# Performance work log

Measured on AMD Instinct MI355X. Metric: run time of the kernel, lower is better.

The kernel has to match this reference:

```python
import jax, jax.numpy as jnp
import numpy as np

B, N, E = 2, 2048, 2048
H, G, D = 16, 4, 128          # num_heads, num_kv_groups, head_dim = E // H
HID = 4 * E                    # GeGLU hidden width
EPS = 1e-6


def setup_inputs() -> dict:
    key = jax.random.key(0)
    ks = jax.random.split(key, 8)
    g = lambda k, shape: jax.random.normal(k, shape, jnp.float32) * 0.02
    return {
        "x": jax.random.normal(ks[0], (B, N, E), jnp.float32),
        "wq": g(ks[1], (E, H * D)),
        "wk": g(ks[2], (E, G * D)),
        "wv": g(ks[3], (E, G * D)),
        "wo": g(ks[4], (H * D, E)),
        "w1": g(ks[5], (E, 2 * HID)),   # GeGLU in-proj (value | gate)
        "w2": g(ks[6], (HID, E)),       # GeGLU out-proj
        "norm1_w": jnp.ones((E,), jnp.float32),
        "norm2_w": jnp.ones((E,), jnp.float32),
    }


def _rope_cos_sin(n, d, dtype):
    inv_freq = 1.0 / (10000.0 ** (jnp.arange(0, d, 2, dtype=jnp.float32) / d))
    freqs = jnp.arange(n, dtype=jnp.float32)[:, None] * inv_freq[None, :]  # [n, d/2]
    emb = jnp.concatenate([freqs, freqs], axis=-1)                          # [n, d]
    return jnp.cos(emb).astype(dtype), jnp.sin(emb).astype(dtype)


def _rotate_half(t):
    d2 = t.shape[-1] // 2
    return jnp.concatenate([-t[..., d2:], t[..., :d2]], axis=-1)


def _apply_rope(t, cos, sin):
    # t: [b, h, n, d]; cos/sin: [n, d]
    return t * cos + _rotate_half(t) * sin


def _rmsnorm(x, w):
    var = jnp.mean(jnp.square(x), axis=-1, keepdims=True)
    return x * jax.lax.rsqrt(var + EPS) * w


def reference(x, wq, wk, wv, wo, w1, w2, norm1_w, norm2_w):
    b, n, _ = x.shape
    # q = k = v = x reshaped into heads (pre-projection, as in source)
    qkv = x.reshape(b, n, H, D).transpose(0, 2, 1, 3)  # [b, H, n, D]
    cos, sin = _rope_cos_sin(n, D, x.dtype)
    q_r = _apply_rope(qkv, cos, sin)
    k_r = _apply_rope(qkv, cos, sin)
    # flatten back to [b, n, E]
    q_flat = q_r.transpose(0, 2, 1, 3).reshape(b, n, E)
    k_flat = k_r.transpose(0, 2, 1, 3).reshape(b, n, E)
    v_flat = x  # v untouched by RoPE; flatten == x

    # Grouped-query attention with internal projections
    qh = (q_flat @ wq).reshape(b, n, H, D).transpose(0, 2, 1, 3)       # [b, H, n, D]
    kh = (k_flat @ wk).reshape(b, n, G, D)                              # [b, n, G, D]
    vh = (v_flat @ wv).reshape(b, n, G, D)
    kh = jnp.repeat(kh, H // G, axis=2).transpose(0, 2, 1, 3)           # [b, H, n, D]
    vh = jnp.repeat(vh, H // G, axis=2).transpose(0, 2, 1, 3)

    scale = 1.0 / np.sqrt(D)
    scores = jnp.einsum('bhqd,bhkd->bhqk', qh, kh) * scale
    attn = jax.nn.softmax(scores, axis=-1)                               # [b, H, n, n]
    ctx = jnp.einsum('bhqk,bhkd->bhqd', attn, vh)
    attn_out = ctx.transpose(0, 2, 1, 3).reshape(b, n, H * D) @ wo      # [b, n, E]

    x1 = _rmsnorm(x + attn_out, norm1_w)

    # GeGLU FFN
    uv = x1 @ w1
    u, gate = jnp.split(uv, 2, axis=-1)
    fc = (u * jax.nn.gelu(gate)) @ w2

    x2 = _rmsnorm(x1 + fc, norm2_w)
    return (x2, (k_flat, v_flat), attn)
```

## Files before the change

### kernel.cpp

```cpp
#include <hip/hip_runtime.h>
#include <hip/hip_bf16.h>


using f32x4  = __attribute__((ext_vector_type(4))) float;
using bf16x8 = __attribute__((ext_vector_type(8))) short;
using bf16x4 = __attribute__((ext_vector_type(4))) short;
using u16x4  = __attribute__((ext_vector_type(4))) unsigned short;

#define DEV __device__ __forceinline__

#define ASYNC16(lds, g)                                                        \
  __builtin_amdgcn_global_load_lds(                                           \
      (const __attribute__((address_space(1))) void*)(g),                      \
      (__attribute__((address_space(3))) void*)(lds), 16, 0, 0)

DEV unsigned short f2bf(float f) {
  unsigned int u = __float_as_uint(f);
  return (unsigned short)((u + 0x7fffu + ((u >> 16) & 1u)) >> 16);
}
DEV float bf2f(unsigned short h) {
  return __uint_as_float(((unsigned int)h) << 16);
}

DEV float waveRedSum(float v) {
#pragma unroll
  for (int o = 32; o; o >>= 1) v += __shfl_xor(v, o);
  return v;
}

__global__ __launch_bounds__(256) void kconvAll(
    const float* __restrict__ wq, const float* __restrict__ wk,
    const float* __restrict__ wv, const float* __restrict__ wo,
    const float* __restrict__ w1, unsigned short* __restrict__ dst) {
  __shared__ float tile[32][33];
  int bx = blockIdx.x * 32;
  int by = blockIdx.y * 32;
  const float* src; int nsrc, c0;
  if (bx < 2048)      { src = wq; nsrc = 2048;  c0 = bx; }
  else if (bx < 2560) { src = wk; nsrc = 512;   c0 = bx - 2048; }
  else if (bx < 3072) { src = wv; nsrc = 512;   c0 = bx - 2560; }
  else if (bx < 5120) { src = wo; nsrc = 2048;  c0 = bx - 3072; }
  else                { src = w1; nsrc = 16384; c0 = bx - 5120; }
  int tx = threadIdx.x & 31;
  int ty = threadIdx.x >> 5;
#pragma unroll
  for (int i = 0; i < 32; i += 8)
    tile[ty + i][tx] = src[(size_t)(by + ty + i) * nsrc + c0 + tx];
  __syncthreads();
#pragma unroll
  for (int i = 0; i < 32; i += 8)
    dst[(size_t)(bx + ty + i) * 2048 + by + tx] = f2bf(tile[tx][ty + i]);
}

__global__ __launch_bounds__(256) void kconvT(const float* __restrict__ in,
                                              unsigned short* __restrict__ out,
                                              int K, int N) {
  __shared__ float tile[32][33];
  int bx = blockIdx.x * 32;
  int by = blockIdx.y * 32;
  int tx = threadIdx.x & 31;
  int ty = threadIdx.x >> 5;
#pragma unroll
  for (int i = 0; i < 32; i += 8)
    tile[ty + i][tx] = in[(size_t)(by + ty + i) * N + bx + tx];
  __syncthreads();
#pragma unroll
  for (int i = 0; i < 32; i += 8)
    out[(size_t)(bx + ty + i) * K + by + tx] = f2bf(tile[tx][ty + i]);
}

__global__ __launch_bounds__(256) void krope(const float* __restrict__ x,
                                             float* __restrict__ kout,
                                             float* __restrict__ vout,
                                             unsigned short* __restrict__ xq,
                                             unsigned short* __restrict__ xb) {
  int idx = blockIdx.x * 256 + threadIdx.x;
  int f  = idx & 63;
  int h  = (idx >> 6) & 15;
  int bn = idx >> 10;
  int n  = bn & 2047;
  size_t base = (size_t)bn * 2048 + h * 128;
  float inv = exp2f((float)f * (-13.287712379549449f / 64.0f));
  float ang = (float)n * inv;
  float c = cosf(ang), s = sinf(ang);
  float a = x[base + f], b = x[base + f + 64];
  float k1 = a * c - b * s;
  float k2 = b * c + a * s;
  __builtin_nontemporal_store(k1, kout + base + f);
  __builtin_nontemporal_store(k2, kout + base + f + 64);
  xq[base + f]      = f2bf(k1);
  xq[base + f + 64] = f2bf(k2);
  __builtin_nontemporal_store(a, vout + base + f);
  __builtin_nontemporal_store(b, vout + base + f + 64);
  xb[base + f]      = f2bf(a);
  xb[base + f + 64] = f2bf(b);
}

__global__ __launch_bounds__(256) void krms1(const float* __restrict__ x,
                                             const unsigned short* __restrict__ ao,
                                             const float* __restrict__ w,
                                             unsigned short* __restrict__ x1b) {
  size_t row = blockIdx.x;
  const f32x4* xp = (const f32x4*)(x + row * 2048);
  const u16x4* ap = (const u16x4*)(ao + row * 2048);
  int tid = threadIdx.x;
  f32x4 x0 = xp[tid * 2], x1v = xp[tid * 2 + 1];
  u16x4 a0 = ap[tid * 2], a1 = ap[tid * 2 + 1];
  f32x4 t0, t1;
#pragma unroll
  for (int i = 0; i < 4; ++i) {
    t0[i] = x0[i] + bf2f(a0[i]);
    t1[i] = x1v[i] + bf2f(a1[i]);
  }
  float ss = 0.f;
#pragma unroll
  for (int i = 0; i < 4; ++i) ss += t0[i] * t0[i] + t1[i] * t1[i];
  ss = waveRedSum(ss);
  __shared__ float red[4];
  int wid = tid >> 6, lane = tid & 63;
  if (!lane) red[wid] = ss;
  __syncthreads();
  ss = red[0] + red[1] + red[2] + red[3];
  float rr = rsqrtf(ss * (1.0f / 2048.0f) + 1e-6f);
  const f32x4* wp = (const f32x4*)w;
  f32x4 w0 = wp[tid * 2], w1 = wp[tid * 2 + 1];
  u16x4 o0, o1;
#pragma unroll
  for (int i = 0; i < 4; ++i) {
    o0[i] = f2bf(t0[i] * rr * w0[i]);
    o1[i] = f2bf(t1[i] * rr * w1[i]);
  }
  u16x4* op = (u16x4*)(x1b + row * 2048);
  op[tid * 2] = o0;
  op[tid * 2 + 1] = o1;
}

__global__ __launch_bounds__(256) void krms2(const unsigned short* __restrict__ x1b,
                                             const unsigned short* __restrict__ fc,
                                             const float* __restrict__ w,
                                             float* __restrict__ out) {
  size_t row = blockIdx.x;
  const u16x4* xp = (const u16x4*)(x1b + row * 2048);
  const u16x4* fp = (const u16x4*)(fc + row * 2048);
  int tid = threadIdx.x;
  u16x4 a0 = xp[tid * 2], a1 = xp[tid * 2 + 1];
  u16x4 b0 = fp[tid * 2], b1 = fp[tid * 2 + 1];
  f32x4 t0, t1;
#pragma unroll
  for (int i = 0; i < 4; ++i) {
    t0[i] = bf2f(a0[i]) + bf2f(b0[i]);
    t1[i] = bf2f(a1[i]) + bf2f(b1[i]);
  }
  float ss = 0.f;
#pragma unroll
  for (int i = 0; i < 4; ++i) ss += t0[i] * t0[i] + t1[i] * t1[i];
  ss = waveRedSum(ss);
  __shared__ float red[4];
  int wid = tid >> 6, lane = tid & 63;
  if (!lane) red[wid] = ss;
  __syncthreads();
  ss = red[0] + red[1] + red[2] + red[3];
  float rr = rsqrtf(ss * (1.0f / 2048.0f) + 1e-6f);
  const f32x4* wp = (const f32x4*)w;
  f32x4 w0 = wp[tid * 2], w1 = wp[tid * 2 + 1];
  f32x4* op = (f32x4*)(out + row * 2048);
  f32x4 o0 = t0 * rr * w0;
  f32x4 o1 = t1 * rr * w1;
  __builtin_nontemporal_store(o0, op + tid * 2);
  __builtin_nontemporal_store(o1, op + tid * 2 + 1);
}

__global__ __launch_bounds__(256, 2) void kvproj(
    const unsigned short* __restrict__ xq, const unsigned short* __restrict__ xb,
    const unsigned short* __restrict__ wkT, const unsigned short* __restrict__ wvT,
    unsigned short* __restrict__ kh, unsigned short* __restrict__ vhT) {
  const bool isV = blockIdx.z != 0;
  const unsigned short* A  = isV ? xb : xq;
  const unsigned short* Bt = isV ? wvT : wkT;
  __shared__ unsigned short As[2][128 * 32];
  __shared__ unsigned short Bs[2][128 * 32];
  const int tid = threadIdx.x;
  const int bm0 = blockIdx.y * 128, bn0 = blockIdx.x * 128;

  f32x4 acc[4][4] = {};

  const int lane = tid & 63, wid = tid >> 6;
  const int wr = wid >> 1, wc = wid & 1;
  const int lr = lane & 15, kq = lane >> 4;

  int srow[2], scc[2];
#pragma unroll
  for (int R = 0; R < 2; ++R) {
    int slot = R * 256 + tid;
    srow[R] = slot >> 2;
    scc[R]  = (slot & 3) ^ (srow[R] & 3);
  }
  auto stage = [&](int buf, int k0) {
#pragma unroll
    for (int R = 0; R < 2; ++R)
      ASYNC16(&As[buf][(R * 256 + tid) * 8],
              A + (size_t)(bm0 + srow[R]) * 2048 + k0 + scc[R] * 8);
#pragma unroll
    for (int R = 0; R < 2; ++R)
      ASYNC16(&Bs[buf][(R * 256 + tid) * 8],
              Bt + (size_t)(bn0 + srow[R]) * 2048 + k0 + scc[R] * 8);
  };

  const int NT = 64;
  stage(0, 0);
  stage(1, 32);
  int cur = 0;
  for (int t = 0; t < NT; ++t) {
    if (t + 1 < NT) asm volatile("s_waitcnt vmcnt(4)" ::: "memory");
    else            asm volatile("s_waitcnt vmcnt(0)" ::: "memory");
    __builtin_amdgcn_sched_barrier(0);
    __builtin_amdgcn_s_barrier();
    __builtin_amdgcn_sched_barrier(0);
    const unsigned short* Ac = As[cur];
    const unsigned short* Bc = Bs[cur];
    bf16x8 afr[4], bfr[4];
#pragma unroll
    for (int i = 0; i < 4; ++i) {
      int row = wr * 64 + i * 16 + lr;
      afr[i] = *(const bf16x8*)&Ac[row * 32 + ((kq ^ (row & 3)) * 8)];
    }
#pragma unroll
    for (int j = 0; j < 4; ++j) {
      int brow = wc * 64 + j * 16 + lr;
      bfr[j] = *(const bf16x8*)&Bc[brow * 32 + ((kq ^ (brow & 3)) * 8)];
    }
    asm volatile("s_waitcnt lgkmcnt(0)" ::: "memory");
    __builtin_amdgcn_sched_barrier(0);
    __builtin_amdgcn_s_barrier();
    __builtin_amdgcn_sched_barrier(0);
    if (t + 2 < NT) stage(cur, (t + 2) * 32);
    __builtin_amdgcn_s_setprio(1);
#pragma unroll
    for (int i = 0; i < 4; ++i)
#pragma unroll
      for (int j = 0; j < 4; ++j)
        acc[i][j] = __builtin_amdgcn_mfma_f32_16x16x32_bf16(afr[i], bfr[j],
                                                            acc[i][j], 0, 0, 0);
    __builtin_amdgcn_s_setprio(0);
    cur ^= 1;
  }

#pragma unroll
  for (int i = 0; i < 4; ++i)
#pragma unroll
    for (int j = 0; j < 4; ++j) {
      int rowb = bm0 + wr * 64 + i * 16 + kq * 4;
      int col = bn0 + wc * 64 + j * 16 + lr;
#pragma unroll
      for (int r = 0; r < 4; ++r) {
        unsigned short v = f2bf(acc[i][j][r]);
        if (isV) vhT[(size_t)col * 4096 + (rowb + r)] = v;
        else     kh[(size_t)(rowb + r) * 512 + col] = v;
      }
    }
}

__global__ __launch_bounds__(512, 4) void kattn(
    const unsigned short* __restrict__ qh,
    const unsigned short* __restrict__ kh,
    const unsigned short* __restrict__ vT,
    float* __restrict__ attn,
    unsigned short* __restrict__ ctx) {
  __shared__ __align__(16) char U[65536];
  __shared__ __align__(16) char Vb[16384];
  float* redm = (float*)Vb;
  float* reds = redm + 128;

  const int tid = threadIdx.x;
  const int lane = tid & 63, w = tid >> 6;
  const int lr = lane & 15, kq = lane >> 4;
  const int bid = blockIdx.x;
  const int g8 = bid & 7;
  const int j  = bid >> 3;
  const int bz = g8 >> 2;
  const int gz = g8 & 3;
  const int hz = gz * 4 + (j & 3);
  const int q0 = (j >> 2) << 4;
  const int z  = bz * 16 + hz;

  const unsigned short* Aq =
      qh + ((size_t)(bz * 2048 + q0 + lr) * 2048 + hz * 128);
  bf16x8 qfr[4];
#pragma unroll
  for (int kk = 0; kk < 4; ++kk)
    qfr[kk] = *(const bf16x8*)(Aq + kk * 32 + kq * 8);

  const unsigned short* Kb =
      kh + ((size_t)(bz * 2048) * 512 + gz * 128);
  int krow[4], kcs[4];
#pragma unroll
  for (int R = 0; R < 4; ++R) {
    int idx = R * 64 + lane;
    krow[R] = idx >> 4;
    kcs[R] = (idx & 15) ^ (krow[R] & 7);
  }
  auto stageK = [&](int buf, int t) {
#pragma unroll
    for (int R = 0; R < 4; ++R)
      ASYNC16(U + buf * 32768 + w * 4096 + (R * 64 + lane) * 16,
              Kb + (size_t)(t * 128 + w * 16 + krow[R]) * 512 + kcs[R] * 8);
  };

  f32x4 acc[16];
#pragma unroll
  for (int t = 0; t < 16; ++t) acc[t] = f32x4{0.f, 0.f, 0.f, 0.f};

  stageK(0, 0);
  stageK(1, 1);
#pragma unroll
  for (int t = 0; t < 16; ++t) {
    if (t < 15) asm volatile("s_waitcnt vmcnt(4)" ::: "memory");
    else        asm volatile("s_waitcnt vmcnt(0)" ::: "memory");
    __builtin_amdgcn_sched_barrier(0);
    const char* Kw = U + (t & 1) * 32768 + w * 4096;
    bf16x8 kfr[4];
#pragma unroll
    for (int kk = 0; kk < 4; ++kk) {
      int cch = (kk * 4 + kq) ^ (lr & 7);
      kfr[kk] = *(const bf16x8*)(Kw + lr * 256 + cch * 16);
    }
    asm volatile("s_waitcnt lgkmcnt(0)" ::: "memory");
    __builtin_amdgcn_sched_barrier(0);
    if (t + 2 < 16) stageK(t & 1, t + 2);
    __builtin_amdgcn_s_setprio(1);
#pragma unroll
    for (int kk = 0; kk < 4; ++kk)
      acc[t] = __builtin_amdgcn_mfma_f32_16x16x32_bf16(kfr[kk], qfr[kk],
                                                       acc[t], 0, 0, 0);
    __builtin_amdgcn_s_setprio(0);
  }

  const float scale = 0.08838834764831845f;
  float mx = -3.4e38f;
#pragma unroll
  for (int t = 0; t < 16; ++t) {
    acc[t] *= scale;
#pragma unroll
    for (int r = 0; r < 4; ++r) mx = fmaxf(mx, acc[t][r]);
  }
  mx = fmaxf(mx, __shfl_xor(mx, 16));
  mx = fmaxf(mx, __shfl_xor(mx, 32));
  float sm = 0.f;
#pragma unroll
  for (int t = 0; t < 16; ++t) {
#pragma unroll
    for (int r = 0; r < 4; ++r) {
      float e = __expf(acc[t][r] - mx);
      acc[t][r] = e;
      sm += e;
    }
  }
  sm += __shfl_xor(sm, 16);
  sm += __shfl_xor(sm, 32);
  if (kq == 0) { redm[w * 16 + lr] = mx; reds[w * 16 + lr] = sm; }
  __syncthreads();
  float m = redm[lr];
#pragma unroll
  for (int ww = 1; ww < 8; ++ww) m = fmaxf(m, redm[ww * 16 + lr]);
  float s = 0.f;
#pragma unroll
  for (int ww = 0; ww < 8; ++ww)
    s += reds[ww * 16 + lr] * __expf(redm[ww * 16 + lr] - m);
  float invw = __expf(mx - m) / s;

  float* arow = attn + (((size_t)z * 2048 + q0 + lr) * 2048);
#pragma unroll
  for (int t = 0; t < 16; ++t) {
    int key = t * 128 + w * 16 + kq * 4;
    f32x4 p = acc[t] * invw;
    __builtin_nontemporal_store(p, (f32x4*)(arow + key));
    bf16x4 pb;
#pragma unroll
    for (int r = 0; r < 4; ++r) pb[r] = (short)f2bf(p[r]);
    int c8 = key >> 3;
    *(bf16x4*)(U + lr * 4096 + ((c8 ^ (lr & 7)) << 4) + ((key & 7) << 1)) = pb;
  }
  __syncthreads();

  const unsigned short* Bv = vT + (size_t)gz * 524288 + bz * 2048;
  const int d0 = w * 16;
  const int vd = lane >> 2;
  const int vcs = (lane & 3) ^ (vd & 3);
  auto stageV = [&](int buf, int t) {
    ASYNC16(Vb + buf * 8192 + w * 1024 + lane * 16,
            Bv + (size_t)(d0 + vd) * 4096 + t * 32 + vcs * 8);
  };

  f32x4 cfr = {};
  stageV(0, 0);
  stageV(1, 1);
#pragma unroll
  for (int t = 0; t < 64; ++t) {
    if (t < 63) asm volatile("s_waitcnt vmcnt(1)" ::: "memory");
    else        asm volatile("s_waitcnt vmcnt(0)" ::: "memory");
    __builtin_amdgcn_sched_barrier(0);
    int c8 = t * 4 + kq;
    bf16x8 pfr = *(const bf16x8*)(U + lr * 4096 + ((c8 ^ (lr & 7)) << 4));
    const char* Vw = Vb + (t & 1) * 8192 + w * 1024;
    bf16x8 vfr = *(const bf16x8*)(Vw + lr * 64 + ((kq ^ (lr & 3)) << 4));
    asm volatile("s_waitcnt lgkmcnt(0)" ::: "memory");
    __builtin_amdgcn_sched_barrier(0);
    if (t + 2 < 64) stageV(t & 1, t + 2);
    __builtin_amdgcn_s_setprio(1);
    cfr = __builtin_amdgcn_mfma_f32_16x16x32_bf16(pfr, vfr, cfr, 0, 0, 0);
    __builtin_amdgcn_s_setprio(0);
  }
#pragma unroll
  for (int r = 0; r < 4; ++r) {
    int q = kq * 4 + r;
    ctx[((size_t)(bz * 2048 + q0 + q) * 2048) + hz * 128 + d0 + lr] =
        f2bf(cfr[r]);
  }
}

template <bool OUT_BF16>
__global__ __launch_bounds__(512, 2) void gemm128(
    const unsigned short* __restrict__ A, const unsigned short* __restrict__ Bt,
    void* __restrict__ C_, int K, int lda, int ldb, int ldc) {
  __shared__ unsigned short As[2][128 * 64];
  __shared__ unsigned short Bs[2][128 * 64];
  const int tid = threadIdx.x;
  const int bid = blockIdx.x;
  const int xcd = bid & 7, ii = bid >> 3;
  const int my = (xcd >> 1) * 8 + (ii & 7);
  const int nx = (xcd & 1) * 8 + (ii >> 3);
  const int bm0 = my * 128, bn0 = nx * 128;
  const int lane = tid & 63, wid = tid >> 6;
  const int wr = wid >> 2, wc = wid & 3;
  const int lr = lane & 15, kq = lane >> 4;

  f32x4 acc[4][2] = {};

  int sArow[2], sAcc[2];
#pragma unroll
  for (int R = 0; R < 2; ++R) {
    int c = R * 512 + tid;
    sArow[R] = c >> 3;
    sAcc[R]  = (c & 7) ^ (sArow[R] & 7);
  }

  auto stage = [&](int buf, int k0) {
#pragma unroll
    for (int R = 0; R < 2; ++R)
      ASYNC16(&As[buf][(R * 512 + tid) * 8],
              A + (size_t)(bm0 + sArow[R]) * lda + k0 + sAcc[R] * 8);
#pragma unroll
    for (int R = 0; R < 2; ++R)
      ASYNC16(&Bs[buf][(R * 512 + tid) * 8],
              Bt + (size_t)(bn0 + sArow[R]) * ldb + k0 + sAcc[R] * 8);
  };

  const int NT = K >> 6;
  stage(0, 0);
  stage(1, 64);
  int cur = 0;
  for (int t = 0; t < NT; ++t) {
    if (t + 1 < NT) asm volatile("s_waitcnt vmcnt(4)" ::: "memory");
    else            asm volatile("s_waitcnt vmcnt(0)" ::: "memory");
    __builtin_amdgcn_sched_barrier(0);
    __builtin_amdgcn_s_barrier();
    __builtin_amdgcn_sched_barrier(0);
    const unsigned short* Ac = As[cur];
    const unsigned short* Bc = Bs[cur];
    bf16x8 afr0[4], bfr0[2];
#pragma unroll
    for (int i = 0; i < 4; ++i) {
      int row = wr * 64 + i * 16 + lr;
      afr0[i] = *(const bf16x8*)&Ac[(row * 8 + (kq ^ (row & 7))) * 8];
    }
#pragma unroll
    for (int j2 = 0; j2 < 2; ++j2) {
      int brow = wc * 32 + j2 * 16 + lr;
      bfr0[j2] = *(const bf16x8*)&Bc[(brow * 8 + (kq ^ (brow & 7))) * 8];
    }
    __builtin_amdgcn_s_setprio(1);
#pragma unroll
    for (int j2 = 0; j2 < 2; ++j2)
#pragma unroll
      for (int i = 0; i < 4; ++i)
        acc[i][j2] = __builtin_amdgcn_mfma_f32_16x16x32_bf16(afr0[i], bfr0[j2],
                                                             acc[i][j2], 0, 0, 0);
    __builtin_amdgcn_s_setprio(0);
    bf16x8 afr1[4], bfr1[2];
#pragma unroll
    for (int i = 0; i < 4; ++i) {
      int row = wr * 64 + i * 16 + lr;
      afr1[i] = *(const bf16x8*)&Ac[(row * 8 + ((4 + kq) ^ (row & 7))) * 8];
    }
#pragma unroll
    for (int j2 = 0; j2 < 2; ++j2) {
      int brow = wc * 32 + j2 * 16 + lr;
      bfr1[j2] = *(const bf16x8*)&Bc[(brow * 8 + ((4 + kq) ^ (brow & 7))) * 8];
    }
    asm volatile("s_waitcnt lgkmcnt(0)" ::: "memory");
    __builtin_amdgcn_sched_barrier(0);
    __builtin_amdgcn_s_barrier();
    __builtin_amdgcn_sched_barrier(0);
    if (t + 2 < NT) stage(cur, (t + 2) << 6);
    __builtin_amdgcn_s_setprio(1);
#pragma unroll
    for (int j2 = 0; j2 < 2; ++j2)
#pragma unroll
      for (int i = 0; i < 4; ++i)
        acc[i][j2] = __builtin_amdgcn_mfma_f32_16x16x32_bf16(afr1[i], bfr1[j2],
                                                             acc[i][j2], 0, 0, 0);
    __builtin_amdgcn_s_setprio(0);
    cur ^= 1;
  }

#pragma unroll
  for (int i = 0; i < 4; ++i)
#pragma unroll
    for (int j = 0; j < 2; ++j) {
      int rowb = bm0 + wr * 64 + i * 16 + kq * 4;
      int col = bn0 + wc * 32 + j * 16 + lr;
#pragma unroll
      for (int r = 0; r < 4; ++r) {
        if constexpr (OUT_BF16)
          ((unsigned short*)C_)[(size_t)(rowb + r) * ldc + col] = f2bf(acc[i][j][r]);
        else
          ((float*)C_)[(size_t)(rowb + r) * ldc + col] = acc[i][j][r];
      }
    }
}

__global__ __launch_bounds__(512, 2) void gemm_geglu256(
    const unsigned short* __restrict__ A, const unsigned short* __restrict__ B1,
    const unsigned short* __restrict__ B2, unsigned short* __restrict__ H_,
    int K, int lda, int ldb, int ldc) {
  __shared__ unsigned short As[2][256 * 64];
  __shared__ unsigned short B1s[2][128 * 64];
  __shared__ unsigned short B2s[2][128 * 64];
  const int tid = threadIdx.x;
  const int bid = blockIdx.x;
  const int xcd = bid & 7, ii = bid >> 3;
  const int my = (xcd >> 2) * 8 + (ii & 7);
  const int nx = (xcd & 3) * 16 + (ii >> 3);
  const int bm0 = my * 256, bn0 = nx * 128;
  const int lane = tid & 63, wid = tid >> 6;
  const int wr = wid >> 2, wc = wid & 3;
  const int lr = lane & 15, kq = lane >> 4;

  f32x4 accu[8][2] = {};
  f32x4 accg[8][2] = {};

  int sArow[4], sAcc[4], sBrow[2], sBcc[2];
#pragma unroll
  for (int R = 0; R < 4; ++R) {
    int c = R * 512 + tid;
    sArow[R] = c >> 3;
    sAcc[R]  = (c & 7) ^ (sArow[R] & 7);
  }
#pragma unroll
  for (int R = 0; R < 2; ++R) {
    int c = R * 512 + tid;
    sBrow[R] = c >> 3;
    sBcc[R]  = (c & 7) ^ (sBrow[R] & 7);
  }

  auto stage = [&](int buf, int k0) {
#pragma unroll
    for (int R = 0; R < 4; ++R)
      ASYNC16(&As[buf][(R * 512 + tid) * 8],
              A + (size_t)(bm0 + sArow[R]) * lda + k0 + sAcc[R] * 8);
#pragma unroll
    for (int R = 0; R < 2; ++R)
      ASYNC16(&B1s[buf][(R * 512 + tid) * 8],
              B1 + (size_t)(bn0 + sBrow[R]) * ldb + k0 + sBcc[R] * 8);
#pragma unroll
    for (int R = 0; R < 2; ++R)
      ASYNC16(&B2s[buf][(R * 512 + tid) * 8],
              B2 + (size_t)(bn0 + sBrow[R]) * ldb + k0 + sBcc[R] * 8);
  };

  const int NT = K >> 6;
  stage(0, 0);
  stage(1, 64);
  int cur = 0;
  for (int t = 0; t < NT; ++t) {
    if (t + 1 < NT) asm volatile("s_waitcnt vmcnt(8)" ::: "memory");
    else            asm volatile("s_waitcnt vmcnt(0)" ::: "memory");
    __builtin_amdgcn_sched_barrier(0);
    __builtin_amdgcn_s_barrier();
    __builtin_amdgcn_sched_barrier(0);
    const unsigned short* Ac = As[cur];
    const unsigned short* B1c = B1s[cur];
    const unsigned short* B2c = B2s[cur];
    bf16x8 afr0[8], b10[2], b20[2];
#pragma unroll
    for (int i = 0; i < 8; ++i) {
      int row = wr * 128 + i * 16 + lr;
      afr0[i] = *(const bf16x8*)&Ac[(row * 8 + (kq ^ (row & 7))) * 8];
    }
#pragma unroll
    for (int j2 = 0; j2 < 2; ++j2) {
      int brow = wc * 32 + j2 * 16 + lr;
      b10[j2] = *(const bf16x8*)&B1c[(brow * 8 + (kq ^ (brow & 7))) * 8];
      b20[j2] = *(const bf16x8*)&B2c[(brow * 8 + (kq ^ (brow & 7))) * 8];
    }
    __builtin_amdgcn_s_setprio(1);
#pragma unroll
    for (int j2 = 0; j2 < 2; ++j2)
#pragma unroll
      for (int i = 0; i < 8; ++i) {
        accu[i][j2] = __builtin_amdgcn_mfma_f32_16x16x32_bf16(afr0[i], b10[j2],
                                                              accu[i][j2], 0, 0, 0);
        accg[i][j2] = __builtin_amdgcn_mfma_f32_16x16x32_bf16(afr0[i], b20[j2],
                                                              accg[i][j2], 0, 0, 0);
      }
    __builtin_amdgcn_s_setprio(0);
    bf16x8 afr1[8], b11[2], b21[2];
#pragma unroll
    for (int i = 0; i < 8; ++i) {
      int row = wr * 128 + i * 16 + lr;
      afr1[i] = *(const bf16x8*)&Ac[(row * 8 + ((4 + kq) ^ (row & 7))) * 8];
    }
#pragma unroll
    for (int j2 = 0; j2 < 2; ++j2) {
      int brow = wc * 32 + j2 * 16 + lr;
      b11[j2] = *(const bf16x8*)&B1c[(brow * 8 + ((4 + kq) ^ (brow & 7))) * 8];
      b21[j2] = *(const bf16x8*)&B2c[(brow * 8 + ((4 + kq) ^ (brow & 7))) * 8];
    }
    asm volatile("s_waitcnt lgkmcnt(0)" ::: "memory");
    __builtin_amdgcn_sched_barrier(0);
    __builtin_amdgcn_s_barrier();
    __builtin_amdgcn_sched_barrier(0);
    if (t + 2 < NT) stage(cur, (t + 2) << 6);
    __builtin_amdgcn_s_setprio(1);
#pragma unroll
    for (int j2 = 0; j2 < 2; ++j2)
#pragma unroll
      for (int i = 0; i < 8; ++i) {
        accu[i][j2] = __builtin_amdgcn_mfma_f32_16x16x32_bf16(afr1[i], b11[j2],
                                                              accu[i][j2], 0, 0, 0);
        accg[i][j2] = __builtin_amdgcn_mfma_f32_16x16x32_bf16(afr1[i], b21[j2],
                                                              accg[i][j2], 0, 0, 0);
      }
    __builtin_amdgcn_s_setprio(0);
    cur ^= 1;
  }

#pragma unroll
  for (int i = 0; i < 8; ++i)
#pragma unroll
    for (int j = 0; j < 2; ++j) {
      int rowb = bm0 + wr * 128 + i * 16 + kq * 4;
      int col = bn0 + wc * 32 + j * 16 + lr;
#pragma unroll
      for (int r = 0; r < 4; ++r) {
        float u = accu[i][j][r];
        float g = accg[i][j][r];
        float tv = tanhf(0.7978845608028654f * (g + 0.044715f * g * g * g));
        float hv = u * 0.5f * g * (1.0f + tv);
        H_[(size_t)(rowb + r) * ldc + col] = f2bf(hv);
      }
    }
}

extern "C" void kernel_launch(void* const* d_in, const int* in_sizes, int n_in,
                              void* d_out, int out_size, void* d_ws, size_t ws_size,
                              hipStream_t stream) {
  const float* x   = (const float*)d_in[0];
  const float* wq  = (const float*)d_in[1];
  const float* wk  = (const float*)d_in[2];
  const float* wv  = (const float*)d_in[3];
  const float* wo  = (const float*)d_in[4];
  const float* w1  = (const float*)d_in[5];
  const float* w2  = (const float*)d_in[6];
  const float* n1w = (const float*)d_in[7];
  const float* n2w = (const float*)d_in[8];

  float* out    = (float*)d_out;
  float* x2_out = out;
  float* k_out  = out + 8388608;
  float* v_out  = out + 16777216;
  float* attn   = out + 25165824;

  char* ws = (char*)d_ws;
  unsigned short* wqT  = (unsigned short*)(ws + 0);
  unsigned short* wkT  = (unsigned short*)(ws + 8388608);
  unsigned short* wvT  = (unsigned short*)(ws + 10485760);
  unsigned short* woT  = (unsigned short*)(ws + 12582912);
  unsigned short* w1T  = (unsigned short*)(ws + 20971520);
  unsigned short* w2T  = (unsigned short*)(ws + 88080384);
  unsigned short* qh   = (unsigned short*)(ws + 121634816);
  unsigned short* kh   = (unsigned short*)(ws + 138412032);
  unsigned short* vhT  = (unsigned short*)(ws + 142606336);
  unsigned short* ctx  = (unsigned short*)(ws + 146800640);
  unsigned short* aob  = (unsigned short*)(ws + 163577856);
  unsigned short* hbuf = (unsigned short*)(ws + 121634816);
  unsigned short* x1b  = (unsigned short*)(ws + 197132288);
  unsigned short* fc   = (unsigned short*)(ws + 213909504);

  unsigned short* xb = (unsigned short*)attn;
  unsigned short* xq = xb + 8388608;

  dim3 blk(256);
  dim3 blk512(512);

  kconvAll<<<dim3(672, 64), blk, 0, stream>>>(wq, wk, wv, wo, w1, wqT);
  kconvT<<<dim3(64, 256), blk, 0, stream>>>(w2, w2T, 8192, 2048);

  krope<<<16384, blk, 0, stream>>>(x, k_out, v_out, xq, xb);

  gemm128<true><<<dim3(512), blk512, 0, stream>>>(
      xq, wqT, qh, 2048, 2048, 2048, 2048);
  kvproj<<<dim3(4, 32, 2), blk, 0, stream>>>(xq, xb, wkT, wvT, kh, vhT);

  kattn<<<dim3(4096), blk512, 0, stream>>>(qh, kh, vhT, attn, ctx);

  gemm128<true><<<dim3(512), blk512, 0, stream>>>(
      ctx, woT, aob, 2048, 2048, 2048, 2048);
  krms1<<<4096, blk, 0, stream>>>(x, aob, n1w, x1b);
  gemm_geglu256<<<dim3(1024), blk512, 0, stream>>>(
      x1b, w1T, w1T + 16777216, hbuf, 2048, 2048, 2048, 8192);
  gemm128<true><<<dim3(512), blk512, 0, stream>>>(
      hbuf, w2T, fc, 8192, 8192, 8192, 2048);
  krms2<<<4096, blk, 0, stream>>>(x1b, fc, n2w, x2_out);
}
```

Before: 905.0 us.

## Merge weight conversion and RoPE kernels; fuse Q/K/V projections into one GEMM

The weight transpose/convert kernels and the RoPE kernel are merged into one launch that dispatches on block index. The Q projection (formerly gemm128) and the K/V projection are merged into a single 768-block GEMM kernel with 512 threads, a 64-wide K tile and an XCD-aware tile mapping for the Q part. The aim is to cut launch overhead and fill the GPU better, because the small K/V GEMM now runs alongside the Q GEMM instead of after it. The risk is that the fused GEMM uses a different tiling from the tuned gemm128, and that the larger LDS footprint may lower occupancy.

```diff
diff --git a/kernel.cpp b/kernel.cpp
--- a/kernel.cpp
+++ b/kernel.cpp
@@ -28,72 +28,69 @@
   return v;
 }
 
-__global__ __launch_bounds__(256) void kconvAll(
+__global__ __launch_bounds__(256) void kprep(
     const float* __restrict__ wq, const float* __restrict__ wk,
     const float* __restrict__ wv, const float* __restrict__ wo,
-    const float* __restrict__ w1, unsigned short* __restrict__ dst) {
+    const float* __restrict__ w1, const float* __restrict__ w2,
+    unsigned short* __restrict__ dst, unsigned short* __restrict__ w2T,
+    const float* __restrict__ x, float* __restrict__ kout,
+    float* __restrict__ vout, unsigned short* __restrict__ xq,
+    unsigned short* __restrict__ xb) {
   __shared__ float tile[32][33];
-  int bx = blockIdx.x * 32;
-  int by = blockIdx.y * 32;
-  const float* src; int nsrc, c0;
-  if (bx < 2048)      { src = wq; nsrc = 2048;  c0 = bx; }
-  else if (bx < 2560) { src = wk; nsrc = 512;   c0 = bx - 2048; }
-  else if (bx < 3072) { src = wv; nsrc = 512;   c0 = bx - 2560; }
-  else if (bx < 5120) { src = wo; nsrc = 2048;  c0 = bx - 3072; }
-  else                { src = w1; nsrc = 16384; c0 = bx - 5120; }
-  int tx = threadIdx.x & 31;
-  int ty = threadIdx.x >> 5;
-#pragma unroll
-  for (int i = 0; i < 32; i += 8)
-    tile[ty + i][tx] = src[(size_t)(by + ty + i) * nsrc + c0 + tx];
-  __syncthreads();
-#pragma unroll
-  for (int i = 0; i < 32; i += 8)
-    dst[(size_t)(bx + ty + i) * 2048 + by + tx] = f2bf(tile[tx][ty + i]);
-}
-
-__global__ __launch_bounds__(256) void kconvT(const float* __restrict__ in,
-                                              unsigned short* __restrict__ out,
-                                              int K, int N) {
-  __shared__ float tile[32][33];
-  int bx = blockIdx.x * 32;
-  int by = blockIdx.y * 32;
-  int tx = threadIdx.x & 31;
-  int ty = threadIdx.x >> 5;
-#pragma unroll
-  for (int i = 0; i < 32; i += 8)
-    tile[ty + i][tx] = in[(size_t)(by + ty + i) * N + bx + tx];
-  __syncthreads();
-#pragma unroll
-  for (int i = 0; i < 32; i += 8)
-    out[(size_t)(bx + ty + i) * K + by + tx] = f2bf(tile[tx][ty + i]);
-}
-
-__global__ __launch_bounds__(256) void krope(const float* __restrict__ x,
-                                             float* __restrict__ kout,
-                                             float* __restrict__ vout,
-                                             unsigned short* __restrict__ xq,
-                                             unsigned short* __restrict__ xb) {
-  int idx = blockIdx.x * 256 + threadIdx.x;
-  int f  = idx & 63;
-  int h  = (idx >> 6) & 15;
-  int bn = idx >> 10;
-  int n  = bn & 2047;
-  size_t base = (size_t)bn * 2048 + h * 128;
-  float inv = exp2f((float)f * (-13.287712379549449f / 64.0f));
-  float ang = (float)n * inv;
-  float c = cosf(ang), s = sinf(ang);
-  float a = x[base + f], b = x[base + f + 64];
-  float k1 = a * c - b * s;
-  float k2 = b * c + a * s;
-  __builtin_nontemporal_store(k1, kout + base + f);
-  __builtin_nontemporal_store(k2, kout + base + f + 64);
-  xq[base + f]      = f2bf(k1);
-  xq[base + f + 64] = f2bf(k2);
-  __builtin_nontemporal_store(a, vout + base + f);
-  __builtin_nontemporal_store(b, vout + base + f + 64);
-  xb[base + f]      = f2bf(a);
-  xb[base + f + 64] = f2bf(b);
+  const int bidg = blockIdx.x;
+  if (bidg < 43008) {
+    int bx = (bidg % 672) * 32;
+    int by = (bidg / 672) * 32;
+    const float* src; int nsrc, c0;
+    if (bx < 2048)      { src = wq; nsrc = 2048;  c0 = bx; }
+    else if (bx < 2560) { src = wk; nsrc = 512;   c0 = bx - 2048; }
+    else if (bx < 3072) { src = wv; nsrc = 512;   c0 = bx - 2560; }
+    else if (bx < 5120) { src = wo; nsrc = 2048;  c0 = bx - 3072; }
+    else                { src = w1; nsrc = 16384; c0 = bx - 5120; }
+    int tx = threadIdx.x & 31;
+    int ty = threadIdx.x >> 5;
+#pragma unroll
+    for (int i = 0; i < 32; i += 8)
+      tile[ty + i][tx] = src[(size_t)(by + ty + i) * nsrc + c0 + tx];
+    __syncthreads();
+#pragma unroll
+    for (int i = 0; i < 32; i += 8)
+      dst[(size_t)(bx + ty + i) * 2048 + by + tx] = f2bf(tile[tx][ty + i]);
+  } else if (bidg < 59392) {
+    int l = bidg - 43008;
+    int bx = (l & 63) * 32;
+    int by = (l >> 6) * 32;
+    int tx = threadIdx.x & 31;
+    int ty = threadIdx.x >> 5;
+#pragma unroll
+    for (int i = 0; i < 32; i += 8)
+      tile[ty + i][tx] = w2[(size_t)(by + ty + i) * 2048 + bx + tx];
+    __syncthreads();
+#pragma unroll
+    for (int i = 0; i < 32; i += 8)
+      w2T[(size_t)(bx + ty + i) * 8192 + by + tx] = f2bf(tile[tx][ty + i]);
+  } else {
+    int idx = (bidg - 59392) * 256 + threadIdx.x;
+    int f  = idx & 63;
+    int h  = (idx >> 6) & 15;
+    int bn = idx >> 10;
+    int n  = bn & 2047;
+    size_t base = (size_t)bn * 2048 + h * 128;
+    float inv = exp2f((float)f * (-13.287712379549449f / 64.0f));
+    float ang = (float)n * inv;
+    float c = cosf(ang), s = sinf(ang);
+    float a = x[base + f], b = x[base + f + 64];
+    float k1 = a * c - b * s;
+    float k2 = b * c + a * s;
+    __builtin_nontemporal_store(k1, kout + base + f);
+    __builtin_nontemporal_store(k2, kout + base + f + 64);
+    xq[base + f]      = f2bf(k1);
+    xq[base + f + 64] = f2bf(k2);
+    __builtin_nontemporal_store(a, vout + base + f);
+    __builtin_nontemporal_store(b, vout + base + f + 64);
+    xb[base + f]      = f2bf(a);
+    xb[base + f + 64] = f2bf(b);
+  }
 }
 
 __global__ __launch_bounds__(256) void krms1(const float* __restrict__ x,
@@ -170,45 +167,61 @@
   __builtin_nontemporal_store(o1, op + tid * 2 + 1);
 }
 
-__global__ __launch_bounds__(256, 2) void kvproj(
+__global__ __launch_bounds__(512, 2) void qkvgemm(
     const unsigned short* __restrict__ xq, const unsigned short* __restrict__ xb,
-    const unsigned short* __restrict__ wkT, const unsigned short* __restrict__ wvT,
+    const unsigned short* __restrict__ wqT, const unsigned short* __restrict__ wkT,
+    const unsigned short* __restrict__ wvT, unsigned short* __restrict__ qh,
     unsigned short* __restrict__ kh, unsigned short* __restrict__ vhT) {
-  const bool isV = blockIdx.z != 0;
-  const unsigned short* A  = isV ? xb : xq;
-  const unsigned short* Bt = isV ? wvT : wkT;
-  __shared__ unsigned short As[2][128 * 32];
-  __shared__ unsigned short Bs[2][128 * 32];
+  __shared__ unsigned short As[2][128 * 64];
+  __shared__ unsigned short Bs[2][128 * 64];
   const int tid = threadIdx.x;
-  const int bm0 = blockIdx.y * 128, bn0 = blockIdx.x * 128;
-
-  f32x4 acc[4][4] = {};
-
+  const int bid = blockIdx.x;
+  const unsigned short *A, *Bt;
+  int bm0, bn0, mode;
+  if (bid < 512) {
+    const int xcd = bid & 7, ii = bid >> 3;
+    bm0 = ((xcd >> 1) * 8 + (ii & 7)) * 128;
+    bn0 = ((xcd & 1) * 8 + (ii >> 3)) * 128;
+    A = xq; Bt = wqT; mode = 0;
+  } else if (bid < 640) {
+    int l = bid - 512;
+    bm0 = (l >> 2) * 128;
+    bn0 = (l & 3) * 128;
+    A = xq; Bt = wkT; mode = 1;
+  } else {
+    int l = bid - 640;
+    bm0 = (l >> 2) * 128;
+    bn0 = (l & 3) * 128;
+    A = xb; Bt = wvT; mode = 2;
+  }
   const int lane = tid & 63, wid = tid >> 6;
-  const int wr = wid >> 1, wc = wid & 1;
+  const int wr = wid >> 2, wc = wid & 3;
   const int lr = lane & 15, kq = lane >> 4;
 
-  int srow[2], scc[2];
+  f32x4 acc[4][2] = {};
+
+  int sArow[2], sAcc[2];
 #pragma unroll
   for (int R = 0; R < 2; ++R) {
-    int slot = R * 256 + tid;
-    srow[R] = slot >> 2;
-    scc[R]  = (slot & 3) ^ (srow[R] & 3);
-  }
+    int c = R * 512 + tid;
+    sArow[R] = c >> 3;
+    sAcc[R]  = (c & 7) ^ (sArow[R] & 7);
+  }
+
   auto stage = [&](int buf, int k0) {
 #pragma unroll
     for (int R = 0; R < 2; ++R)
-      ASYNC16(&As[buf][(R * 256 + tid) * 8],
-              A + (size_t)(bm0 + srow[R]) * 2048 + k0 + scc[R] * 8);
+      ASYNC16(&As[buf][(R * 512 + tid) * 8],
+              A + (size_t)(bm0 + sArow[R]) * 2048 + k0 + sAcc[R] * 8);
 #pragma unroll
     for (int R = 0; R < 2; ++R)
-      ASYNC16(&Bs[buf][(R * 256 + tid) * 8],
-              Bt + (size_t)(bn0 + srow[R]) * 2048 + k0 + scc[R] * 8);
+      ASYNC16(&Bs[buf][(R * 512 + tid) * 8],
+              Bt + (size_t)(bn0 + sArow[R]) * 2048 + k0 + sAcc[R] * 8);
   };
 
-  const int NT = 64;
+  const int NT = 32;
   stage(0, 0);
-  stage(1, 32);
+  stage(1, 64);
   int cur = 0;
   for (int t = 0; t < NT; ++t) {
     if (t + 1 < NT) asm volatile("s_waitcnt vmcnt(4)" ::: "memory");
@@ -218,29 +231,48 @@
     __builtin_amdgcn_sched_barrier(0);
     const unsigned short* Ac = As[cur];
     const unsigned short* Bc = Bs[cur];
-    bf16x8 afr[4], bfr[4];
+    bf16x8 afr0[4], bfr0[2];
 #pragma unroll
     for (int i = 0; i < 4; ++i) {
       int row = wr * 64 + i * 16 + lr;
-      afr[i] = *(const bf16x8*)&Ac[row * 32 + ((kq ^ (row & 3)) * 8)];
-    }
-#pragma unroll
-    for (int j = 0; j < 4; ++j) {
-      int brow = wc * 64 + j * 16 + lr;
-      bfr[j] = *(const bf16x8*)&Bc[brow * 32 + ((kq ^ (brow & 3)) * 8)];
+      afr0[i] = *(const bf16x8*)&Ac[(row * 8 + (kq ^ (row & 7))) * 8];
+    }
+#pragma unroll
+    for (int j2 = 0; j2 < 2; ++j2) {
+      int brow = wc * 32 + j2 * 16 + lr;
+      bfr0[j2] = *(const bf16x8*)&Bc[(brow * 8 + (kq ^ (brow & 7))) * 8];
+    }
+    __builtin_amdgcn_s_setprio(1);
+#pragma unroll
+    for (int j2 = 0; j2 < 2; ++j2)
+#pragma unroll
+      for (int i = 0; i < 4; ++i)
+        acc[i][j2] = __builtin_amdgcn_mfma_f32_16x16x32_bf16(afr0[i], bfr0[j2],
+                                                             acc[i][j2], 0, 0, 0);
+    __builtin_amdgcn_s_setprio(0);
+    bf16x8 afr1[4], bfr1[2];
+#pragma unroll
+    for (int i = 0; i < 4; ++i) {
+      int row = wr * 64 + i * 16 + lr;
+      afr1[i] = *(const bf16x8*)&Ac[(row * 8 + ((4 + kq) ^ (row & 7))) * 8];
+    }
+#pragma unroll
+    for (int j2 = 0; j2 < 2; ++j2) {
+      int brow = wc * 32 + j2 * 16 + lr;
+      bfr1[j2] = *(const bf16x8*)&Bc[(brow * 8 + ((4 + kq) ^ (brow & 7))) * 8];
     }
     asm volatile("s_waitcnt lgkmcnt(0)" ::: "memory");
     __builtin_amdgcn_sched_barrier(0);
     __builtin_amdgcn_s_barrier();
     __builtin_amdgcn_sched_barrier(0);
-    if (t + 2 < NT) stage(cur, (t + 2) * 32);
+    if (t + 2 < NT) stage(cur, (t + 2) << 6);
     __builtin_amdgcn_s_setprio(1);
 #pragma unroll
-    for (int i = 0; i < 4; ++i)
-#pragma unroll
-      for (int j = 0; j < 4; ++j)
-        acc[i][j] = __builtin_amdgcn_mfma_f32_16x16x32_bf16(afr[i], bfr[j],
-                                                            acc[i][j], 0, 0, 0);
+    for (int j2 = 0; j2 < 2; ++j2)
+#pragma unroll
+      for (int i = 0; i < 4; ++i)
+        acc[i][j2] = __builtin_amdgcn_mfma_f32_16x16x32_bf16(afr1[i], bfr1[j2],
+                                                             acc[i][j2], 0, 0, 0);
     __builtin_amdgcn_s_setprio(0);
     cur ^= 1;
   }
@@ -248,14 +280,15 @@
 #pragma unroll
   for (int i = 0; i < 4; ++i)
 #pragma unroll
-    for (int j = 0; j < 4; ++j) {
+    for (int j = 0; j < 2; ++j) {
       int rowb = bm0 + wr * 64 + i * 16 + kq * 4;
-      int col = bn0 + wc * 64 + j * 16 + lr;
+      int col = bn0 + wc * 32 + j * 16 + lr;
 #pragma unroll
       for (int r = 0; r < 4; ++r) {
         unsigned short v = f2bf(acc[i][j][r]);
-        if (isV) vhT[(size_t)col * 4096 + (rowb + r)] = v;
-        else     kh[(size_t)(rowb + r) * 512 + col] = v;
+        if (mode == 0)      qh[(size_t)(rowb + r) * 2048 + col] = v;
+        else if (mode == 1) kh[(size_t)(rowb + r) * 512 + col] = v;
+        else                vhT[(size_t)col * 4096 + (rowb + r)] = v;
       }
     }
 }
@@ -703,14 +736,10 @@
   dim3 blk(256);
   dim3 blk512(512);
 
-  kconvAll<<<dim3(672, 64), blk, 0, stream>>>(wq, wk, wv, wo, w1, wqT);
-  kconvT<<<dim3(64, 256), blk, 0, stream>>>(w2, w2T, 8192, 2048);
-
-  krope<<<16384, blk, 0, stream>>>(x, k_out, v_out, xq, xb);
-
-  gemm128<true><<<dim3(512), blk512, 0, stream>>>(
-      xq, wqT, qh, 2048, 2048, 2048, 2048);
-  kvproj<<<dim3(4, 32, 2), blk, 0, stream>>>(xq, xb, wkT, wvT, kh, vhT);
+  kprep<<<dim3(75776), blk, 0, stream>>>(wq, wk, wv, wo, w1, w2, wqT, w2T,
+                                         x, k_out, v_out, xq, xb);
+
+  qkvgemm<<<dim3(768), blk512, 0, stream>>>(xq, xb, wqT, wkT, wvT, qh, kh, vhT);
 
   kattn<<<dim3(4096), blk512, 0, stream>>>(qh, kh, vhT, attn, ctx);
 
```

Measured after the change: 903.1 us. About the same (-0.2%).
